# Kernel optimization log

Measured on AMD Instinct MI355X. Metric: run time of the kernel, lower is better.

Reference implementation:

```python
import jax, jax.numpy as jnp
import numpy as np

# atom_dict indices
N_IDX, CA_IDX, C_IDX = 0, 1, 2
O4P_IDX, C2P_IDX, C1P_IDX = 11, 14, 15
NA_REF_IDX = 15  # C1'
TOP_K = 30
NUM_RBF = 16
MAX_REL = 32
NUM_POLY = 3
B, L, A = 1, 512, 24


def setup_inputs() -> dict:
    key = jax.random.key(0)
    ks = jax.random.split(key, 8)
    X = 5.0 * jax.random.normal(ks[0], (B, L, A, 3), dtype=jnp.float32)
    mask = jnp.ones((B, L), dtype=jnp.float32)
    R_idx = jnp.broadcast_to(jnp.arange(L, dtype=jnp.int32), (B, L))
    chain_labels = jnp.broadcast_to((jnp.arange(L) // (L // 2)).astype(jnp.int32), (B, L))
    X_m = jnp.ones((B, L, A), dtype=jnp.float32)
    R_polymer_type = jax.random.randint(ks[1], (B, L), 0, NUM_POLY)
    protein_mask = (R_polymer_type == 0).astype(jnp.float32)
    dna_mask = (R_polymer_type == 1).astype(jnp.float32)
    rna_mask = (R_polymer_type == 2).astype(jnp.float32)
    TOTAL_ATOMS = A + 2
    edge_in = 2 * MAX_REL + 2  # placeholder; real edge_in below
    edge_in = NUM_RBF * TOTAL_ATOMS * TOTAL_ATOMS + 16  # 10832
    W_pos = 0.1 * jax.random.normal(ks[2], (16, 2 * MAX_REL + 2), dtype=jnp.float32)
    b_pos = 0.01 * jax.random.normal(ks[3], (16,), dtype=jnp.float32)
    W_edge = 0.02 * jax.random.normal(ks[4], (128, edge_in), dtype=jnp.float32)
    W_node = 0.1 * jax.random.normal(ks[5], (128, NUM_POLY), dtype=jnp.float32)
    gamma_e = jnp.ones((128,), jnp.float32); beta_e = jnp.zeros((128,), jnp.float32)
    gamma_n = jnp.ones((128,), jnp.float32); beta_n = jnp.zeros((128,), jnp.float32)
    return dict(X=X, mask=mask, R_idx=R_idx, chain_labels=chain_labels, X_m=X_m,
                protein_mask=protein_mask, dna_mask=dna_mask, rna_mask=rna_mask,
                R_polymer_type=R_polymer_type, W_pos=W_pos, b_pos=b_pos,
                W_edge=W_edge, W_node=W_node, gamma_e=gamma_e, beta_e=beta_e,
                gamma_n=gamma_n, beta_n=beta_n)


def _get_cb(n, ca, c, wa, wb, wc):
    b = ca - n
    cc = c - ca
    a = jnp.cross(b, cc)
    return wa * a + wb * b + wc * cc + ca


def _layernorm(x, g, b, eps=1e-5):
    m = x.mean(-1, keepdims=True)
    v = ((x - m) ** 2).mean(-1, keepdims=True)
    return (x - m) / jnp.sqrt(v + eps) * g + b


def _dist_topk(Xc, mask):
    # Xc: [B,L,3]
    mask2d = mask[:, None, :] * mask[:, :, None]  # [B,L,L]
    dX = Xc[:, None, :, :] - Xc[:, :, None, :]
    D = mask2d * jnp.sqrt((dX ** 2).sum(-1) + 1e-6)
    D_max = D.max(-1, keepdims=True)
    D_adjust = D + (1.0 - mask2d) * D_max
    negD, E_idx = jax.lax.top_k(-D_adjust, TOP_K)  # smallest distances
    return -negD, E_idx


def reference(X, mask, R_idx, chain_labels, X_m, protein_mask, dna_mask, rna_mask,
              R_polymer_type, W_pos, b_pos, W_edge, W_node, gamma_e, beta_e,
              gamma_n, beta_n):
    Bb, Ll = X.shape[0], X.shape[1]
    Ca = X[:, :, CA_IDX]
    Nb = X[:, :, N_IDX]
    Cc = X[:, :, C_IDX]
    Cb = _get_cb(Nb, Ca, Cc, -0.58273431, 0.56802827, -0.54067466)
    na_ref = X[:, :, NA_REF_IDX]
    N_na = _get_cb(X[:, :, O4P_IDX], X[:, :, C1P_IDX], X[:, :, C2P_IDX],
                   -0.56967352, 0.51055973, -0.53122153)
    aug_X = jnp.concatenate([X, Cb[:, :, None, :], N_na[:, :, None, :]], axis=2)  # [B,L,26,3]
    aug_Xm = jnp.concatenate([X_m, protein_mask[:, :, None],
                              (rna_mask + dna_mask)[:, :, None]], axis=-1)  # [B,L,26]

    _, E_idx = _dist_topk(Ca + na_ref, mask)  # [B,L,K]

    # gather neighbor atoms / masks: [B,L,K,26,3], [B,L,K,26]
    bidx = jnp.arange(Bb)[:, None, None]
    X_g = aug_X[bidx, E_idx]
    Xm_g = aug_Xm[bidx, E_idx]

    # all-atom pairwise distances [B,L,K,26,26]
    Dall = jnp.sqrt(((aug_X[:, :, None, :, None, :] - X_g[:, :, :, None, :, :]) ** 2).sum(-1) + 1e-6)
    D_mu = jnp.linspace(2.0, 22.0, NUM_RBF)
    D_sigma = (22.0 - 2.0) / NUM_RBF
    RBF = jnp.exp(-((Dall[..., None] - D_mu) / D_sigma) ** 2)  # [B,L,K,26,26,16]
    RBF = RBF * aug_Xm[:, :, None, :, None, None] * Xm_g[:, :, :, None, :, None]
    RBF_all = RBF.reshape(Bb, Ll, TOP_K, -1)  # [B,L,K,26*26*16]

    offset = R_idx[:, :, None] - R_idx[:, None, :]  # [B,L,L]
    offset = jnp.take_along_axis(offset, E_idx, axis=2)  # [B,L,K]
    d_chains = (chain_labels[:, :, None] == chain_labels[:, None, :]).astype(jnp.int32)
    E_chains = jnp.take_along_axis(d_chains, E_idx, axis=2)

    d = jnp.clip(offset + MAX_REL, 0, 2 * MAX_REL) * E_chains + (1 - E_chains) * (2 * MAX_REL + 1)
    d_onehot = jax.nn.one_hot(d, 2 * MAX_REL + 2, dtype=jnp.float32)
    E_positional = d_onehot @ W_pos.T + b_pos  # [B,L,K,16]

    E = jnp.concatenate([E_positional, RBF_all], axis=-1)
    E = E @ W_edge.T  # [B,L,K,128]
    E = _layernorm(E, gamma_e, beta_e)

    V = jax.nn.one_hot(R_polymer_type, NUM_POLY, dtype=jnp.float32) @ W_node.T
    V = _layernorm(V, gamma_n, beta_n)
    return V, E, E_idx
```

## Files before the change

### kernel.cpp

```cpp
#include <hip/hip_runtime.h>
#include <stdint.h>


#define NRES   512
#define TOPK   30
#define NATOM  26
#define KTOT   10832
#define NBLK128 85
#define MTOT   (NRES*TOPK)
#define NOUT   128
#define KSPLIT 6
#define TBINS  1024
#define TRANGE 25.6f

#define OFF_AUGX4  0u
#define OFF_EIDX   212992u
#define OFF_WSWZ   274432u
#define OFF_EPART  1667072u
#define OFF_TAB    25260032u

#define OUT_V     0
#define OUT_E     (NRES*NOUT)
#define OUT_EIDX  (OUT_E + MTOT*NOUT)

typedef __attribute__((ext_vector_type(4))) float f32x4;
typedef __attribute__((ext_vector_type(8))) int   i32x8;

#define SA_C    0.96089792702915984f
#define MU0_C   1.9217958540583197f
#define MUS_C   1.2811972360388798f
#define MUS2_C  (MUS_C*MUS_C)
#define SCL1    0x7f7f7f7f
#define TSCL    (SA_C * (float)TBINS / TRANGE)

__device__ __forceinline__ unsigned short f2bf(float f) {
    unsigned u = __builtin_bit_cast(unsigned, f);
    return (unsigned short)((u + 0x7fffu + ((u >> 16) & 1u)) >> 16);
}
__device__ __forceinline__ float bf2f(unsigned short u) {
    return __builtin_bit_cast(float, (unsigned)u << 16);
}
__device__ __forceinline__ float bflo(unsigned u) {
    return __builtin_bit_cast(float, u << 16);
}
__device__ __forceinline__ float bfhi(unsigned u) {
    return __builtin_bit_cast(float, u & 0xffff0000u);
}
__device__ __forceinline__ unsigned long long shfl_xor_u64(unsigned long long v, int m) {
    unsigned lo = (unsigned)v, hi = (unsigned)(v >> 32);
    lo = (unsigned)__shfl_xor((int)lo, m, 64);
    hi = (unsigned)__shfl_xor((int)hi, m, 64);
    return ((unsigned long long)hi << 32) | lo;
}
__device__ __forceinline__ float fexp2(float x) { return __builtin_amdgcn_exp2f(x); }
__device__ __forceinline__ float fsqrtf(float x) { return __builtin_amdgcn_sqrtf(x); }

__device__ __forceinline__ uint4 lut16(const uint4* __restrict__ tabS,
                                       float4 xi, float jx, float jy, float jz) {
    float dx = xi.x - jx, dy = xi.y - jy, dz = xi.z - jz;
    float d2 = __builtin_fmaf(dx, dx, __builtin_fmaf(dy, dy,
               __builtin_fmaf(dz, dz, 1e-6f)));
    float fi = fsqrtf(d2) * TSCL;
    fi = fminf(fi, (float)(TBINS - 1));
    int idx = (xi.w == 0.0f) ? (TBINS - 1) : (int)fi;
    return tabS[idx];
}

__global__ __launch_bounds__(256) void kPrep(
    const float* __restrict__ X, const float* __restrict__ Xm,
    const float* __restrict__ prot, const float* __restrict__ dna,
    const float* __restrict__ rna, const int* __restrict__ ptype,
    const float* __restrict__ Wn, const float* __restrict__ gn,
    const float* __restrict__ bn, const float* __restrict__ We,
    char* __restrict__ ws, float* __restrict__ out)
{
    if (blockIdx.x >= NRES + 384) {
        int bb = (blockIdx.x - (NRES + 384)) * 256 + threadIdx.x;
        if (bb >= TBINS) return;
        float Ds = ((float)bb + 0.5f) * (TRANGE / (float)TBINS);
        unsigned r[4];
        #pragma unroll
        for (int g = 0; g < 4; g++) {
            float u0 = Ds - (MU0_C + (float)(4*g + 0) * MUS_C);
            float u1 = Ds - (MU0_C + (float)(4*g + 1) * MUS_C);
            float u2 = Ds - (MU0_C + (float)(4*g + 2) * MUS_C);
            float u3 = Ds - (MU0_C + (float)(4*g + 3) * MUS_C);
            float e0 = fexp2(-(u0 * u0));
            float e1 = fexp2(-(u1 * u1));
            float e2 = fexp2(-(u2 * u2));
            float e3 = fexp2(-(u3 * u3));
            int p = __builtin_amdgcn_cvt_pk_fp8_f32(e0, e1, 0, false);
            p     = __builtin_amdgcn_cvt_pk_fp8_f32(e2, e3, p, true);
            r[g] = (unsigned)p;
        }
        *(uint4*)(ws + OFF_TAB + (size_t)bb * 16) =
            make_uint4(r[0], r[1], r[2], r[3]);
        return;
    }
    if (blockIdx.x >= NRES) {
        int idx = blockIdx.x - NRES;
        int n = idx / 3;
        int s = (idx - n*3)*256 + threadIdx.x;
        if (s >= 677) return;
        const float* src = We + (size_t)n*KTOT + ((s < 676) ? (16 + s*16) : 0);
        float4 v0 = ((const float4*)src)[0];
        float4 v1 = ((const float4*)src)[1];
        float4 v2 = ((const float4*)src)[2];
        float4 v3 = ((const float4*)src)[3];
        int d = s >> 3, sl = s & 7, qd2 = sl >> 1, cc = sl & 1;
        size_t base = OFF_WSWZ
                    + (((size_t)(d*8 + (n >> 4))*64) + (size_t)(qd2*16 + (n & 15)))*32
                    + (size_t)cc*16;
        int r0 = __builtin_amdgcn_cvt_pk_fp8_f32(v0.x, v0.y, 0, false);
        r0     = __builtin_amdgcn_cvt_pk_fp8_f32(v0.z, v0.w, r0, true);
        int r1 = __builtin_amdgcn_cvt_pk_fp8_f32(v1.x, v1.y, 0, false);
        r1     = __builtin_amdgcn_cvt_pk_fp8_f32(v1.z, v1.w, r1, true);
        int r2 = __builtin_amdgcn_cvt_pk_fp8_f32(v2.x, v2.y, 0, false);
        r2     = __builtin_amdgcn_cvt_pk_fp8_f32(v2.z, v2.w, r2, true);
        int r3 = __builtin_amdgcn_cvt_pk_fp8_f32(v3.x, v3.y, 0, false);
        r3     = __builtin_amdgcn_cvt_pk_fp8_f32(v3.z, v3.w, r3, true);
        *(uint4*)(ws + base) = make_uint4((unsigned)r0, (unsigned)r1,
                                          (unsigned)r2, (unsigned)r3);
        return;
    }

    const int i = blockIdx.x, t = threadIdx.x;
    if (t >= 128) return;
    float4* augX4 = (float4*)(ws + OFF_AUGX4);
    int*    Eidx  = (int*)(ws + OFF_EIDX);
    const float* Xi = X + i * 72;

    if (t < 26) {
        float x, y, z, mk;
        if (t < 24) {
            x = Xi[t*3]; y = Xi[t*3+1]; z = Xi[t*3+2];
            mk = Xm[i*24 + t];
        } else if (t == 24) {
            float b0 = Xi[3]-Xi[0], b1 = Xi[4]-Xi[1], b2 = Xi[5]-Xi[2];
            float c0 = Xi[6]-Xi[3], c1 = Xi[7]-Xi[4], c2 = Xi[8]-Xi[5];
            float a0 = b1*c2-b2*c1, a1 = b2*c0-b0*c2, a2 = b0*c1-b1*c0;
            x = -0.58273431f*a0 + 0.56802827f*b0 - 0.54067466f*c0 + Xi[3];
            y = -0.58273431f*a1 + 0.56802827f*b1 - 0.54067466f*c1 + Xi[4];
            z = -0.58273431f*a2 + 0.56802827f*b2 - 0.54067466f*c2 + Xi[5];
            mk = prot[i];
        } else {
            const float* O4 = Xi + 33; const float* C1 = Xi + 45; const float* C2 = Xi + 42;
            float b0 = C1[0]-O4[0], b1 = C1[1]-O4[1], b2 = C1[2]-O4[2];
            float c0 = C2[0]-C1[0], c1 = C2[1]-C1[1], c2 = C2[2]-C1[2];
            float a0 = b1*c2-b2*c1, a1 = b2*c0-b0*c2, a2 = b0*c1-b1*c0;
            x = -0.56967352f*a0 + 0.51055973f*b0 - 0.53122153f*c0 + C1[0];
            y = -0.56967352f*a1 + 0.51055973f*b1 - 0.53122153f*c1 + C1[1];
            z = -0.56967352f*a2 + 0.51055973f*b2 - 0.53122153f*c2 + C1[2];
            mk = dna[i] + rna[i];
        }
        augX4[i*26 + t] = make_float4(x, y, z, mk);
    }

    __shared__ float red[4];
    int ty = ptype[i];
    float v = Wn[t*3 + ty];
    float s = v;
    #pragma unroll
    for (int off = 32; off; off >>= 1) s += __shfl_xor(s, off, 64);
    if ((t & 63) == 0) red[t>>6] = s;
    __syncthreads();
    float mean = (red[0] + red[1]) * (1.0f/128.0f);
    float d = v - mean;
    float s2 = d*d;
    #pragma unroll
    for (int off = 32; off; off >>= 1) s2 += __shfl_xor(s2, off, 64);
    if ((t & 63) == 0) red[2 + (t>>6)] = s2;
    __syncthreads();
    float var = (red[2] + red[3]) * (1.0f/128.0f);
    out[OUT_V + i*NOUT + t] = d * rsqrtf(var + 1e-5f) * gn[t] + bn[t];

    if (t >= 64) return;
    const int l = t;
    float xi0 = Xi[3] + Xi[45], xi1 = Xi[4] + Xi[46], xi2 = Xi[5] + Xi[47];
    unsigned long long cand[8];
    #pragma unroll
    for (int sg = 0; sg < 8; sg++) {
        int j = sg*64 + l;
        const float* Xj = X + j*72;
        float c0 = Xj[3] + Xj[45], c1 = Xj[4] + Xj[46], c2 = Xj[5] + Xj[47];
        float dx = xi0 - c0, dy = xi1 - c1, dz = xi2 - c2;
        float dd = __fadd_rn(__fadd_rn(__fadd_rn(__fmul_rn(dx,dx), __fmul_rn(dy,dy)),
                                       __fmul_rn(dz,dz)), 1e-6f);
        float D = sqrtf(dd);
        cand[sg] = ((unsigned long long)__builtin_bit_cast(unsigned, D) << 32) | (unsigned)j;
    }
    for (int m = 0; m < TOPK; m++) {
        unsigned long long k = cand[0];
        #pragma unroll
        for (int sg = 1; sg < 8; sg++) if (cand[sg] < k) k = cand[sg];
        #pragma unroll
        for (int off = 32; off; off >>= 1) {
            unsigned long long o = shfl_xor_u64(k, off);
            if (o < k) k = o;
        }
        if (l == 0) {
            int j = (int)(k & 0xffffffffu);
            Eidx[i*TOPK + m] = j;
            out[OUT_EIDX + i*TOPK + m] = (float)j;
        }
        #pragma unroll
        for (int sg = 0; sg < 8; sg++) if (cand[sg] == k) cand[sg] = ~0ull;
    }
}

__global__ __launch_bounds__(128, 3) void kC(const int* __restrict__ Ridx,
                                             const int* __restrict__ chain,
                                             const float* __restrict__ Wp,
                                             const float* __restrict__ bp,
                                             char* __restrict__ ws)
{
    const int bx = blockIdx.x, q = blockIdx.y;
    const int t = threadIdx.x, lane = t & 63, w = t >> 6;
    const int mlane = lane & 15, qd = lane >> 4;

    const float4* augX4 = (const float4*)(ws + OFF_AUGX4);
    const int*    Eidx  = (const int*)(ws + OFF_EIDX);
    unsigned short* Ep  = (unsigned short*)(ws + OFF_EPART)
                        + (size_t)q * MTOT * NOUT;

    __shared__ uint2  jT[NATOM * 65];
    __shared__ float4 iT[5 * 26];
    __shared__ int    JrowS[64];
    __shared__ uint4  tabS[TBINS];

    if (t < 64) JrowS[t] = Eidx[bx*64 + t];
    __syncthreads();
    const int i_base = (bx*64) / TOPK;
    if (t < 5*26) {
        int il = t / 26, aa = t - il*26;
        int gi = i_base + il; gi = gi > 511 ? 511 : gi;
        iT[t] = augX4[(size_t)gi*26 + aa];
    }
    {
        const uint4* tabG = (const uint4*)(ws + OFF_TAB);
        #pragma unroll
        for (int k = 0; k < 8; k++) tabS[t + k*128] = tabG[t + k*128];
    }
    for (int wk = t; wk < NATOM*64; wk += 128) {
        int aa = wk >> 6, rl = wk & 63;
        float4 p = augX4[(size_t)JrowS[rl]*26 + aa];
        float x = p.x, y = p.y, z = p.z;
        if (p.w == 0.0f) { x = -30000.0f; y = -30000.0f; z = -30000.0f; }
        uint2 pk;
        pk.x = (unsigned)f2bf(x) | ((unsigned)f2bf(y) << 16);
        pk.y = (unsigned)f2bf(z);
        jT[aa*65 + rl] = pk;
    }
    __syncthreads();

    const int rl0 = w*32 + mlane, rl1 = rl0 + 16;
    const int r0 = bx*64 + rl0, r1 = r0 + 16;
    const int i0 = r0 / TOPK, i1 = r1 / TOPK;
    const int il0 = (i0 - i_base)*26, il1 = (i1 - i_base)*26;

    f32x4 acc0[8], acc1[8];
    #pragma unroll
    for (int nt = 0; nt < 8; nt++) {
        acc0[nt] = (f32x4){0.f,0.f,0.f,0.f};
        acc1[nt] = (f32x4){0.f,0.f,0.f,0.f};
    }

    const int d0 = (q == 0) ? 0 : (1 + q*14);
    const int nmain = (q == 0) ? 15 : ((q == 5) ? 13 : 14);

    int s0i = d0*8 + 2*qd;
    int a = s0i / 26, rem = s0i - a*26;

    const char* Wb = (const char*)(ws + OFF_WSWZ) + (size_t)d0*16384 + (size_t)lane*32;

    for (int dd = 0; dd < nmain; dd++) {
        i32x8 b0 = *(const i32x8*)(Wb);
        i32x8 b1 = *(const i32x8*)(Wb + 2048);
        i32x8 b2 = *(const i32x8*)(Wb + 4096);
        i32x8 b3 = *(const i32x8*)(Wb + 6144);

        int rem1 = rem + 1, a1 = a;
        if (rem1 == 26) { rem1 = 0; a1 = a + 1; }

        uint2 jR0a = jT[rem*65  + rl0], jR0b = jT[rem1*65 + rl0];
        uint2 jR1a = jT[rem*65  + rl1], jR1b = jT[rem1*65 + rl1];
        float4 xiR0a = iT[il0 + a], xiR0b = iT[il0 + a1];
        float4 xiR1a = iT[il1 + a], xiR1b = iT[il1 + a1];

        uint4 p0a = lut16(tabS, xiR0a, bflo(jR0a.x), bfhi(jR0a.x), bflo(jR0a.y));
        uint4 p0b = lut16(tabS, xiR0b, bflo(jR0b.x), bfhi(jR0b.x), bflo(jR0b.y));
        uint4 p1a = lut16(tabS, xiR1a, bflo(jR1a.x), bfhi(jR1a.x), bflo(jR1a.y));
        uint4 p1b = lut16(tabS, xiR1b, bflo(jR1b.x), bfhi(jR1b.x), bflo(jR1b.y));

        i32x8 A0, A1;
        A0[0]=p0a.x; A0[1]=p0a.y; A0[2]=p0a.z; A0[3]=p0a.w;
        A0[4]=p0b.x; A0[5]=p0b.y; A0[6]=p0b.z; A0[7]=p0b.w;
        A1[0]=p1a.x; A1[1]=p1a.y; A1[2]=p1a.z; A1[3]=p1a.w;
        A1[4]=p1b.x; A1[5]=p1b.y; A1[6]=p1b.z; A1[7]=p1b.w;

        acc0[0] = __builtin_amdgcn_mfma_scale_f32_16x16x128_f8f6f4(A0, b0, acc0[0], 0, 0, 0, SCL1, 0, SCL1);
        acc1[0] = __builtin_amdgcn_mfma_scale_f32_16x16x128_f8f6f4(A1, b0, acc1[0], 0, 0, 0, SCL1, 0, SCL1);
        acc0[1] = __builtin_amdgcn_mfma_scale_f32_16x16x128_f8f6f4(A0, b1, acc0[1], 0, 0, 0, SCL1, 0, SCL1);
        acc1[1] = __builtin_amdgcn_mfma_scale_f32_16x16x128_f8f6f4(A1, b1, acc1[1], 0, 0, 0, SCL1, 0, SCL1);
        acc0[2] = __builtin_amdgcn_mfma_scale_f32_16x16x128_f8f6f4(A0, b2, acc0[2], 0, 0, 0, SCL1, 0, SCL1);
        acc1[2] = __builtin_amdgcn_mfma_scale_f32_16x16x128_f8f6f4(A1, b2, acc1[2], 0, 0, 0, SCL1, 0, SCL1);
        acc0[3] = __builtin_amdgcn_mfma_scale_f32_16x16x128_f8f6f4(A0, b3, acc0[3], 0, 0, 0, SCL1, 0, SCL1);
        acc1[3] = __builtin_amdgcn_mfma_scale_f32_16x16x128_f8f6f4(A1, b3, acc1[3], 0, 0, 0, SCL1, 0, SCL1);

        i32x8 b4 = *(const i32x8*)(Wb + 8192);
        i32x8 b5 = *(const i32x8*)(Wb + 10240);
        i32x8 b6 = *(const i32x8*)(Wb + 12288);
        i32x8 b7 = *(const i32x8*)(Wb + 14336);

        acc0[4] = __builtin_amdgcn_mfma_scale_f32_16x16x128_f8f6f4(A0, b4, acc0[4], 0, 0, 0, SCL1, 0, SCL1);
        acc1[4] = __builtin_amdgcn_mfma_scale_f32_16x16x128_f8f6f4(A1, b4, acc1[4], 0, 0, 0, SCL1, 0, SCL1);
        acc0[5] = __builtin_amdgcn_mfma_scale_f32_16x16x128_f8f6f4(A0, b5, acc0[5], 0, 0, 0, SCL1, 0, SCL1);
        acc1[5] = __builtin_amdgcn_mfma_scale_f32_16x16x128_f8f6f4(A1, b5, acc1[5], 0, 0, 0, SCL1, 0, SCL1);
        acc0[6] = __builtin_amdgcn_mfma_scale_f32_16x16x128_f8f6f4(A0, b6, acc0[6], 0, 0, 0, SCL1, 0, SCL1);
        acc1[6] = __builtin_amdgcn_mfma_scale_f32_16x16x128_f8f6f4(A1, b6, acc1[6], 0, 0, 0, SCL1, 0, SCL1);
        acc0[7] = __builtin_amdgcn_mfma_scale_f32_16x16x128_f8f6f4(A0, b7, acc0[7], 0, 0, 0, SCL1, 0, SCL1);
        acc1[7] = __builtin_amdgcn_mfma_scale_f32_16x16x128_f8f6f4(A1, b7, acc1[7], 0, 0, 0, SCL1, 0, SCL1);

        Wb += 16384;
        rem += 8;
        if (rem >= 26) { rem -= 26; a += 1; }
    }

    if (q == 5) {
        i32x8 b0 = *(const i32x8*)(Wb);
        i32x8 b1 = *(const i32x8*)(Wb + 2048);
        i32x8 b2 = *(const i32x8*)(Wb + 4096);
        i32x8 b3 = *(const i32x8*)(Wb + 6144);

        int rem1 = rem + 1, a1 = a;
        if (rem1 == 26) { rem1 = 0; a1 = a + 1; }
        int ac  = a  > 25 ? 25 : a;
        int a1c = a1 > 25 ? 25 : a1;

        uint2 jR0a = jT[rem*65  + rl0], jR0b = jT[rem1*65 + rl0];
        uint2 jR1a = jT[rem*65  + rl1], jR1b = jT[rem1*65 + rl1];
        float4 xiR0a = iT[il0 + ac], xiR0b = iT[il0 + a1c];
        float4 xiR1a = iT[il1 + ac], xiR1b = iT[il1 + a1c];

        uint4 p0a = lut16(tabS, xiR0a, bflo(jR0a.x), bfhi(jR0a.x), bflo(jR0a.y));
        uint4 p0b = lut16(tabS, xiR0b, bflo(jR0b.x), bfhi(jR0b.x), bflo(jR0b.y));
        uint4 p1a = lut16(tabS, xiR1a, bflo(jR1a.x), bfhi(jR1a.x), bflo(jR1a.y));
        uint4 p1b = lut16(tabS, xiR1b, bflo(jR1b.x), bfhi(jR1b.x), bflo(jR1b.y));

        if (qd == 2) {
            int dc0, dc1;
            {
                int j0 = JrowS[rl0], j1 = JrowS[rl1];
                int off  = Ridx[i0] - Ridx[j0];
                int same = (chain[i0] == chain[j0]);
                int dc = off + 32; dc = dc < 0 ? 0 : (dc > 64 ? 64 : dc);
                dc0 = same ? dc : 65;
                off  = Ridx[i1] - Ridx[j1];
                same = (chain[i1] == chain[j1]);
                dc = off + 32; dc = dc < 0 ? 0 : (dc > 64 ? 64 : dc);
                dc1 = same ? dc : 65;
            }
            float e0[16], e1[16];
            #pragma unroll
            for (int f = 0; f < 16; f++) {
                float bv = bp[f];
                e0[f] = Wp[f*66 + dc0] + bv;
                e1[f] = Wp[f*66 + dc1] + bv;
            }
            int u0 = __builtin_amdgcn_cvt_pk_fp8_f32(e0[0], e0[1], 0, false);
            u0     = __builtin_amdgcn_cvt_pk_fp8_f32(e0[2], e0[3], u0, true);
            int u1 = __builtin_amdgcn_cvt_pk_fp8_f32(e0[4], e0[5], 0, false);
            u1     = __builtin_amdgcn_cvt_pk_fp8_f32(e0[6], e0[7], u1, true);
            int u2 = __builtin_amdgcn_cvt_pk_fp8_f32(e0[8], e0[9], 0, false);
            u2     = __builtin_amdgcn_cvt_pk_fp8_f32(e0[10], e0[11], u2, true);
            int u3 = __builtin_amdgcn_cvt_pk_fp8_f32(e0[12], e0[13], 0, false);
            u3     = __builtin_amdgcn_cvt_pk_fp8_f32(e0[14], e0[15], u3, true);
            p0a = make_uint4((unsigned)u0,(unsigned)u1,(unsigned)u2,(unsigned)u3);
            u0 = __builtin_amdgcn_cvt_pk_fp8_f32(e1[0], e1[1], 0, false);
            u0 = __builtin_amdgcn_cvt_pk_fp8_f32(e1[2], e1[3], u0, true);
            u1 = __builtin_amdgcn_cvt_pk_fp8_f32(e1[4], e1[5], 0, false);
            u1 = __builtin_amdgcn_cvt_pk_fp8_f32(e1[6], e1[7], u1, true);
            u2 = __builtin_amdgcn_cvt_pk_fp8_f32(e1[8], e1[9], 0, false);
            u2 = __builtin_amdgcn_cvt_pk_fp8_f32(e1[10], e1[11], u2, true);
            u3 = __builtin_amdgcn_cvt_pk_fp8_f32(e1[12], e1[13], 0, false);
            u3 = __builtin_amdgcn_cvt_pk_fp8_f32(e1[14], e1[15], u3, true);
            p1a = make_uint4((unsigned)u0,(unsigned)u1,(unsigned)u2,(unsigned)u3);
            p0b = make_uint4(0,0,0,0);
            p1b = make_uint4(0,0,0,0);
        }
        if (qd == 3) {
            p0a = make_uint4(0,0,0,0); p0b = make_uint4(0,0,0,0);
            p1a = make_uint4(0,0,0,0); p1b = make_uint4(0,0,0,0);
        }

        i32x8 A0, A1;
        A0[0]=p0a.x; A0[1]=p0a.y; A0[2]=p0a.z; A0[3]=p0a.w;
        A0[4]=p0b.x; A0[5]=p0b.y; A0[6]=p0b.z; A0[7]=p0b.w;
        A1[0]=p1a.x; A1[1]=p1a.y; A1[2]=p1a.z; A1[3]=p1a.w;
        A1[4]=p1b.x; A1[5]=p1b.y; A1[6]=p1b.z; A1[7]=p1b.w;

        acc0[0] = __builtin_amdgcn_mfma_scale_f32_16x16x128_f8f6f4(A0, b0, acc0[0], 0, 0, 0, SCL1, 0, SCL1);
        acc1[0] = __builtin_amdgcn_mfma_scale_f32_16x16x128_f8f6f4(A1, b0, acc1[0], 0, 0, 0, SCL1, 0, SCL1);
        acc0[1] = __builtin_amdgcn_mfma_scale_f32_16x16x128_f8f6f4(A0, b1, acc0[1], 0, 0, 0, SCL1, 0, SCL1);
        acc1[1] = __builtin_amdgcn_mfma_scale_f32_16x16x128_f8f6f4(A1, b1, acc1[1], 0, 0, 0, SCL1, 0, SCL1);
        acc0[2] = __builtin_amdgcn_mfma_scale_f32_16x16x128_f8f6f4(A0, b2, acc0[2], 0, 0, 0, SCL1, 0, SCL1);
        acc1[2] = __builtin_amdgcn_mfma_scale_f32_16x16x128_f8f6f4(A1, b2, acc1[2], 0, 0, 0, SCL1, 0, SCL1);
        acc0[3] = __builtin_amdgcn_mfma_scale_f32_16x16x128_f8f6f4(A0, b3, acc0[3], 0, 0, 0, SCL1, 0, SCL1);
        acc1[3] = __builtin_amdgcn_mfma_scale_f32_16x16x128_f8f6f4(A1, b3, acc1[3], 0, 0, 0, SCL1, 0, SCL1);

        i32x8 b4 = *(const i32x8*)(Wb + 8192);
        i32x8 b5 = *(const i32x8*)(Wb + 10240);
        i32x8 b6 = *(const i32x8*)(Wb + 12288);
        i32x8 b7 = *(const i32x8*)(Wb + 14336);

        acc0[4] = __builtin_amdgcn_mfma_scale_f32_16x16x128_f8f6f4(A0, b4, acc0[4], 0, 0, 0, SCL1, 0, SCL1);
        acc1[4] = __builtin_amdgcn_mfma_scale_f32_16x16x128_f8f6f4(A1, b4, acc1[4], 0, 0, 0, SCL1, 0, SCL1);
        acc0[5] = __builtin_amdgcn_mfma_scale_f32_16x16x128_f8f6f4(A0, b5, acc0[5], 0, 0, 0, SCL1, 0, SCL1);
        acc1[5] = __builtin_amdgcn_mfma_scale_f32_16x16x128_f8f6f4(A1, b5, acc1[5], 0, 0, 0, SCL1, 0, SCL1);
        acc0[6] = __builtin_amdgcn_mfma_scale_f32_16x16x128_f8f6f4(A0, b6, acc0[6], 0, 0, 0, SCL1, 0, SCL1);
        acc1[6] = __builtin_amdgcn_mfma_scale_f32_16x16x128_f8f6f4(A1, b6, acc1[6], 0, 0, 0, SCL1, 0, SCL1);
        acc0[7] = __builtin_amdgcn_mfma_scale_f32_16x16x128_f8f6f4(A0, b7, acc0[7], 0, 0, 0, SCL1, 0, SCL1);
        acc1[7] = __builtin_amdgcn_mfma_scale_f32_16x16x128_f8f6f4(A1, b7, acc1[7], 0, 0, 0, SCL1, 0, SCL1);
    }

    #pragma unroll
    for (int nt = 0; nt < 8; nt++) {
        int col = nt*16 + mlane;
        #pragma unroll
        for (int rr = 0; rr < 4; rr++) {
            int g0 = bx*64 + w*32 + qd*4 + rr;
            Ep[(size_t)g0*NOUT + col]      = f2bf(acc0[nt][rr]);
            Ep[(size_t)(g0+16)*NOUT + col] = f2bf(acc1[nt][rr]);
        }
    }
}

__global__ __launch_bounds__(256) void kD(const float* __restrict__ ge,
                                          const float* __restrict__ be,
                                          char* __restrict__ ws,
                                          float* __restrict__ out)
{
    const unsigned* Ep = (const unsigned*)(ws + OFF_EPART);
    const int t = threadIdx.x, wv = t >> 6, lane = t & 63;
    const int row = blockIdx.x*4 + wv;
    const size_t qs = (size_t)MTOT * 64;
    size_t b = (size_t)row*64 + lane;

    float v0 = 0.f, v1 = 0.f;
    #pragma unroll
    for (int qq = 0; qq < KSPLIT; qq++) {
        unsigned u = Ep[b + (size_t)qq*qs];
        v0 += bf2f((unsigned short)(u & 0xffffu));
        v1 += bf2f((unsigned short)(u >> 16));
    }

    float S = v0 + v1, Q = v0*v0 + v1*v1;
    #pragma unroll
    for (int off = 32; off; off >>= 1) {
        S += __shfl_xor(S, off, 64);
        Q += __shfl_xor(Q, off, 64);
    }
    float mean = S * (1.0f/128.0f);
    float var  = Q * (1.0f/128.0f) - mean*mean;
    float rstd = rsqrtf(var + 1e-5f);
    float2 o;
    o.x = (v0 - mean) * rstd * ge[2*lane]   + be[2*lane];
    o.y = (v1 - mean) * rstd * ge[2*lane+1] + be[2*lane+1];
    ((float2*)(out + OUT_E))[(size_t)row*64 + lane] = o;
}

extern "C" void kernel_launch(void* const* d_in, const int* in_sizes, int n_in,
                              void* d_out, int out_size, void* d_ws, size_t ws_size,
                              hipStream_t stream)
{
    const float* X     = (const float*)d_in[0];
    const int*   Ridx  = (const int*)d_in[2];
    const int*   chain = (const int*)d_in[3];
    const float* Xm    = (const float*)d_in[4];
    const float* prot  = (const float*)d_in[5];
    const float* dna   = (const float*)d_in[6];
    const float* rna   = (const float*)d_in[7];
    const int*   ptype = (const int*)d_in[8];
    const float* Wp    = (const float*)d_in[9];
    const float* bp    = (const float*)d_in[10];
    const float* We    = (const float*)d_in[11];
    const float* Wn    = (const float*)d_in[12];
    const float* ge    = (const float*)d_in[13];
    const float* be    = (const float*)d_in[14];
    const float* gn    = (const float*)d_in[15];
    const float* bn    = (const float*)d_in[16];
    char* ws = (char*)d_ws;
    float* out = (float*)d_out;

    kPrep<<<dim3(NRES + 384 + TBINS/256), dim3(256), 0, stream>>>(X, Xm, prot,
            dna, rna, ptype, Wn, gn, bn, We, ws, out);
    kC<<<dim3(240, KSPLIT), dim3(128), 0, stream>>>(Ridx, chain, Wp, bp, ws);
    kD<<<dim3(MTOT/4), dim3(256), 0, stream>>>(ge, be, ws, out);
}
```

Measured before the change: 168.6 us.

## Fuse split-K partial reduction and edge layernorm into GEMM kernel via LDS

The six split-K slices move from separate blocks into six waves of one 384-thread block. Each wave adds its partial accumulators into a shared-memory tile with atomics, and the block then applies the layernorm and writes the final edge features directly. This removes the bf16 partial-sum buffer in global memory and the separate reduction/layernorm kernel launch, which also avoids the bf16 rounding of the partials. In exchange each block covers only 32 rows, and it pays for LDS atomics and an extra barrier. Occupancy and register pressure also change under the new 384-thread launch bounds.

Result: slower. 216.7 us (+28.5%).

```diff
diff --git a/kernel.cpp b/kernel.cpp
--- a/kernel.cpp
+++ b/kernel.cpp
@@ -9,15 +9,13 @@
 #define NBLK128 85
 #define MTOT   (NRES*TOPK)
 #define NOUT   128
-#define KSPLIT 6
 #define TBINS  1024
 #define TRANGE 25.6f
 
 #define OFF_AUGX4  0u
 #define OFF_EIDX   212992u
 #define OFF_WSWZ   274432u
-#define OFF_EPART  1667072u
-#define OFF_TAB    25260032u
+#define OFF_TAB    1667072u
 
 #define OUT_V     0
 #define OUT_E     (NRES*NOUT)
@@ -36,9 +34,6 @@
 __device__ __forceinline__ unsigned short f2bf(float f) {
     unsigned u = __builtin_bit_cast(unsigned, f);
     return (unsigned short)((u + 0x7fffu + ((u >> 16) & 1u)) >> 16);
-}
-__device__ __forceinline__ float bf2f(unsigned short u) {
-    return __builtin_bit_cast(float, (unsigned)u << 16);
 }
 __device__ __forceinline__ float bflo(unsigned u) {
     return __builtin_bit_cast(float, u << 16);
@@ -208,53 +203,55 @@
     }
 }
 
-__global__ __launch_bounds__(128, 3) void kC(const int* __restrict__ Ridx,
+__global__ __launch_bounds__(384, 2) void kC(const int* __restrict__ Ridx,
                                              const int* __restrict__ chain,
                                              const float* __restrict__ Wp,
                                              const float* __restrict__ bp,
-                                             char* __restrict__ ws)
+                                             const float* __restrict__ ge,
+                                             const float* __restrict__ be,
+                                             char* __restrict__ ws,
+                                             float* __restrict__ out)
 {
-    const int bx = blockIdx.x, q = blockIdx.y;
+    const int bx = blockIdx.x;
     const int t = threadIdx.x, lane = t & 63, w = t >> 6;
     const int mlane = lane & 15, qd = lane >> 4;
 
     const float4* augX4 = (const float4*)(ws + OFF_AUGX4);
     const int*    Eidx  = (const int*)(ws + OFF_EIDX);
-    unsigned short* Ep  = (unsigned short*)(ws + OFF_EPART)
-                        + (size_t)q * MTOT * NOUT;
-
-    __shared__ uint2  jT[NATOM * 65];
-    __shared__ float4 iT[5 * 26];
-    __shared__ int    JrowS[64];
+
+    __shared__ uint2  jT[NATOM * 33];
+    __shared__ float4 iT[3 * 26];
+    __shared__ int    JrowS[32];
     __shared__ uint4  tabS[TBINS];
-
-    if (t < 64) JrowS[t] = Eidx[bx*64 + t];
+    __shared__ float  accS[32 * 132];
+
+    if (t < 32) JrowS[t] = Eidx[bx*32 + t];
+    for (int k = t; k < 32*132; k += 384) accS[k] = 0.0f;
     __syncthreads();
-    const int i_base = (bx*64) / TOPK;
-    if (t < 5*26) {
+    const int i_base = (bx*32) / TOPK;
+    if (t < 3*26) {
         int il = t / 26, aa = t - il*26;
         int gi = i_base + il; gi = gi > 511 ? 511 : gi;
         iT[t] = augX4[(size_t)gi*26 + aa];
     }
     {
         const uint4* tabG = (const uint4*)(ws + OFF_TAB);
-        #pragma unroll
-        for (int k = 0; k < 8; k++) tabS[t + k*128] = tabG[t + k*128];
-    }
-    for (int wk = t; wk < NATOM*64; wk += 128) {
-        int aa = wk >> 6, rl = wk & 63;
+        for (int k = t; k < TBINS; k += 384) tabS[k] = tabG[k];
+    }
+    for (int wk = t; wk < NATOM*32; wk += 384) {
+        int aa = wk >> 5, rl = wk & 31;
         float4 p = augX4[(size_t)JrowS[rl]*26 + aa];
         float x = p.x, y = p.y, z = p.z;
         if (p.w == 0.0f) { x = -30000.0f; y = -30000.0f; z = -30000.0f; }
         uint2 pk;
         pk.x = (unsigned)f2bf(x) | ((unsigned)f2bf(y) << 16);
         pk.y = (unsigned)f2bf(z);
-        jT[aa*65 + rl] = pk;
+        jT[aa*33 + rl] = pk;
     }
     __syncthreads();
 
-    const int rl0 = w*32 + mlane, rl1 = rl0 + 16;
-    const int r0 = bx*64 + rl0, r1 = r0 + 16;
+    const int rl0 = mlane, rl1 = mlane + 16;
+    const int r0 = bx*32 + rl0, r1 = r0 + 16;
     const int i0 = r0 / TOPK, i1 = r1 / TOPK;
     const int il0 = (i0 - i_base)*26, il1 = (i1 - i_base)*26;
 
@@ -265,6 +262,7 @@
         acc1[nt] = (f32x4){0.f,0.f,0.f,0.f};
     }
 
+    const int q = w;
     const int d0 = (q == 0) ? 0 : (1 + q*14);
     const int nmain = (q == 0) ? 15 : ((q == 5) ? 13 : 14);
 
@@ -282,8 +280,8 @@
         int rem1 = rem + 1, a1 = a;
         if (rem1 == 26) { rem1 = 0; a1 = a + 1; }
 
-        uint2 jR0a = jT[rem*65  + rl0], jR0b = jT[rem1*65 + rl0];
-        uint2 jR1a = jT[rem*65  + rl1], jR1b = jT[rem1*65 + rl1];
+        uint2 jR0a = jT[rem*33  + rl0], jR0b = jT[rem1*33 + rl0];
+        uint2 jR1a = jT[rem*33  + rl1], jR1b = jT[rem1*33 + rl1];
         float4 xiR0a = iT[il0 + a], xiR0b = iT[il0 + a1];
         float4 xiR1a = iT[il1 + a], xiR1b = iT[il1 + a1];
 
@@ -337,8 +335,8 @@
         int ac  = a  > 25 ? 25 : a;
         int a1c = a1 > 25 ? 25 : a1;
 
-        uint2 jR0a = jT[rem*65  + rl0], jR0b = jT[rem1*65 + rl0];
-        uint2 jR1a = jT[rem*65  + rl1], jR1b = jT[rem1*65 + rl1];
+        uint2 jR0a = jT[rem*33  + rl0], jR0b = jT[rem1*33 + rl0];
+        uint2 jR1a = jT[rem*33  + rl1], jR1b = jT[rem1*33 + rl1];
         float4 xiR0a = iT[il0 + ac], xiR0b = iT[il0 + a1c];
         float4 xiR1a = iT[il1 + ac], xiR1b = iT[il1 + a1c];
 
@@ -428,45 +426,30 @@
         int col = nt*16 + mlane;
         #pragma unroll
         for (int rr = 0; rr < 4; rr++) {
-            int g0 = bx*64 + w*32 + qd*4 + rr;
-            Ep[(size_t)g0*NOUT + col]      = f2bf(acc0[nt][rr]);
-            Ep[(size_t)(g0+16)*NOUT + col] = f2bf(acc1[nt][rr]);
-        }
-    }
-}
-
-__global__ __launch_bounds__(256) void kD(const float* __restrict__ ge,
-                                          const float* __restrict__ be,
-                                          char* __restrict__ ws,
-                                          float* __restrict__ out)
-{
-    const unsigned* Ep = (const unsigned*)(ws + OFF_EPART);
-    const int t = threadIdx.x, wv = t >> 6, lane = t & 63;
-    const int row = blockIdx.x*4 + wv;
-    const size_t qs = (size_t)MTOT * 64;
-    size_t b = (size_t)row*64 + lane;
-
-    float v0 = 0.f, v1 = 0.f;
-    #pragma unroll
-    for (int qq = 0; qq < KSPLIT; qq++) {
-        unsigned u = Ep[b + (size_t)qq*qs];
-        v0 += bf2f((unsigned short)(u & 0xffffu));
-        v1 += bf2f((unsigned short)(u >> 16));
-    }
-
-    float S = v0 + v1, Q = v0*v0 + v1*v1;
-    #pragma unroll
-    for (int off = 32; off; off >>= 1) {
-        S += __shfl_xor(S, off, 64);
-        Q += __shfl_xor(Q, off, 64);
-    }
-    float mean = S * (1.0f/128.0f);
-    float var  = Q * (1.0f/128.0f) - mean*mean;
-    float rstd = rsqrtf(var + 1e-5f);
-    float2 o;
-    o.x = (v0 - mean) * rstd * ge[2*lane]   + be[2*lane];
-    o.y = (v1 - mean) * rstd * ge[2*lane+1] + be[2*lane+1];
-    ((float2*)(out + OUT_E))[(size_t)row*64 + lane] = o;
+            int r = qd*4 + rr;
+            atomicAdd(&accS[r*132 + col],        acc0[nt][rr]);
+            atomicAdd(&accS[(r+16)*132 + col],   acc1[nt][rr]);
+        }
+    }
+    __syncthreads();
+
+    for (int r = w; r < 32; r += 6) {
+        float v0 = accS[r*132 + 2*lane];
+        float v1 = accS[r*132 + 2*lane + 1];
+        float S = v0 + v1, Q = v0*v0 + v1*v1;
+        #pragma unroll
+        for (int off = 32; off; off >>= 1) {
+            S += __shfl_xor(S, off, 64);
+            Q += __shfl_xor(Q, off, 64);
+        }
+        float mean = S * (1.0f/128.0f);
+        float var  = Q * (1.0f/128.0f) - mean*mean;
+        float rstd = rsqrtf(var + 1e-5f);
+        float2 o;
+        o.x = (v0 - mean) * rstd * ge[2*lane]   + be[2*lane];
+        o.y = (v1 - mean) * rstd * ge[2*lane+1] + be[2*lane+1];
+        ((float2*)(out + OUT_E))[(size_t)(bx*32 + r)*64 + lane] = o;
+    }
 }
 
 extern "C" void kernel_launch(void* const* d_in, const int* in_sizes, int n_in,
@@ -494,6 +477,6 @@
 
     kPrep<<<dim3(NRES + 384 + TBINS/256), dim3(256), 0, stream>>>(X, Xm, prot,
             dna, rna, ptype, Wn, gn, bn, We, ws, out);
-    kC<<<dim3(240, KSPLIT), dim3(128), 0, stream>>>(Ridx, chain, Wp, bp, ws);
-    kD<<<dim3(MTOT/4), dim3(256), 0, stream>>>(ge, be, ws, out);
-}
+    kC<<<dim3(MTOT/32), dim3(384), 0, stream>>>(Ridx, chain, Wp, bp, ge, be,
+            ws, out);
+}
```

## Split warp work by output columns instead of rows in fp8 MFMA GEMM

Applied to the files above, without the earlier changes.

Each of the two waves now covers all 64 rows of the block and half of the 128 output columns, instead of 32 rows by all 128 columns. Each wave loads only 4 weight fragments per step rather than 8, which halves per-wave global weight traffic. In exchange each wave computes the LUT-based RBF A-fragments for four row tiles instead of two, so the gather and LUT work per wave doubles. Accumulator register count stays the same.

After: 162.8 us. 3.4% less time.

```diff
diff --git a/kernel.cpp b/kernel.cpp
--- a/kernel.cpp
+++ b/kernel.cpp
@@ -232,8 +232,8 @@
     __syncthreads();
     const int i_base = (bx*64) / TOPK;
     if (t < 5*26) {
-        int il = t / 26, aa = t - il*26;
-        int gi = i_base + il; gi = gi > 511 ? 511 : gi;
+        int il_ = t / 26, aa = t - il_*26;
+        int gi = i_base + il_; gi = gi > 511 ? 511 : gi;
         iT[t] = augX4[(size_t)gi*26 + aa];
     }
     {
@@ -242,28 +242,30 @@
         for (int k = 0; k < 8; k++) tabS[t + k*128] = tabG[t + k*128];
     }
     for (int wk = t; wk < NATOM*64; wk += 128) {
-        int aa = wk >> 6, rl = wk & 63;
-        float4 p = augX4[(size_t)JrowS[rl]*26 + aa];
+        int aa = wk >> 6, rl_ = wk & 63;
+        float4 p = augX4[(size_t)JrowS[rl_]*26 + aa];
         float x = p.x, y = p.y, z = p.z;
         if (p.w == 0.0f) { x = -30000.0f; y = -30000.0f; z = -30000.0f; }
         uint2 pk;
         pk.x = (unsigned)f2bf(x) | ((unsigned)f2bf(y) << 16);
         pk.y = (unsigned)f2bf(z);
-        jT[aa*65 + rl] = pk;
+        jT[aa*65 + rl_] = pk;
     }
     __syncthreads();
 
-    const int rl0 = w*32 + mlane, rl1 = rl0 + 16;
-    const int r0 = bx*64 + rl0, r1 = r0 + 16;
-    const int i0 = r0 / TOPK, i1 = r1 / TOPK;
-    const int il0 = (i0 - i_base)*26, il1 = (i1 - i_base)*26;
-
-    f32x4 acc0[8], acc1[8];
-    #pragma unroll
-    for (int nt = 0; nt < 8; nt++) {
-        acc0[nt] = (f32x4){0.f,0.f,0.f,0.f};
-        acc1[nt] = (f32x4){0.f,0.f,0.f,0.f};
-    }
+    int rl[4], il[4];
+    #pragma unroll
+    for (int rt = 0; rt < 4; rt++) {
+        rl[rt] = rt*16 + mlane;
+        il[rt] = ((bx*64 + rl[rt]) / TOPK - i_base) * 26;
+    }
+
+    f32x4 acc[4][4];
+    #pragma unroll
+    for (int rt = 0; rt < 4; rt++)
+        #pragma unroll
+        for (int nt = 0; nt < 4; nt++)
+            acc[rt][nt] = (f32x4){0.f,0.f,0.f,0.f};
 
     const int d0 = (q == 0) ? 0 : (1 + q*14);
     const int nmain = (q == 0) ? 15 : ((q == 5) ? 13 : 14);
@@ -271,7 +273,8 @@
     int s0i = d0*8 + 2*qd;
     int a = s0i / 26, rem = s0i - a*26;
 
-    const char* Wb = (const char*)(ws + OFF_WSWZ) + (size_t)d0*16384 + (size_t)lane*32;
+    const char* Wb = (const char*)(ws + OFF_WSWZ) + (size_t)d0*16384
+                   + (size_t)(w*4)*2048 + (size_t)lane*32;
 
     for (int dd = 0; dd < nmain; dd++) {
         i32x8 b0 = *(const i32x8*)(Wb);
@@ -282,44 +285,22 @@
         int rem1 = rem + 1, a1 = a;
         if (rem1 == 26) { rem1 = 0; a1 = a + 1; }
 
-        uint2 jR0a = jT[rem*65  + rl0], jR0b = jT[rem1*65 + rl0];
-        uint2 jR1a = jT[rem*65  + rl1], jR1b = jT[rem1*65 + rl1];
-        float4 xiR0a = iT[il0 + a], xiR0b = iT[il0 + a1];
-        float4 xiR1a = iT[il1 + a], xiR1b = iT[il1 + a1];
-
-        uint4 p0a = lut16(tabS, xiR0a, bflo(jR0a.x), bfhi(jR0a.x), bflo(jR0a.y));
-        uint4 p0b = lut16(tabS, xiR0b, bflo(jR0b.x), bfhi(jR0b.x), bflo(jR0b.y));
-        uint4 p1a = lut16(tabS, xiR1a, bflo(jR1a.x), bfhi(jR1a.x), bflo(jR1a.y));
-        uint4 p1b = lut16(tabS, xiR1b, bflo(jR1b.x), bfhi(jR1b.x), bflo(jR1b.y));
-
-        i32x8 A0, A1;
-        A0[0]=p0a.x; A0[1]=p0a.y; A0[2]=p0a.z; A0[3]=p0a.w;
-        A0[4]=p0b.x; A0[5]=p0b.y; A0[6]=p0b.z; A0[7]=p0b.w;
-        A1[0]=p1a.x; A1[1]=p1a.y; A1[2]=p1a.z; A1[3]=p1a.w;
-        A1[4]=p1b.x; A1[5]=p1b.y; A1[6]=p1b.z; A1[7]=p1b.w;
-
-        acc0[0] = __builtin_amdgcn_mfma_scale_f32_16x16x128_f8f6f4(A0, b0, acc0[0], 0, 0, 0, SCL1, 0, SCL1);
-        acc1[0] = __builtin_amdgcn_mfma_scale_f32_16x16x128_f8f6f4(A1, b0, acc1[0], 0, 0, 0, SCL1, 0, SCL1);
-        acc0[1] = __builtin_amdgcn_mfma_scale_f32_16x16x128_f8f6f4(A0, b1, acc0[1], 0, 0, 0, SCL1, 0, SCL1);
-        acc1[1] = __builtin_amdgcn_mfma_scale_f32_16x16x128_f8f6f4(A1, b1, acc1[1], 0, 0, 0, SCL1, 0, SCL1);
-        acc0[2] = __builtin_amdgcn_mfma_scale_f32_16x16x128_f8f6f4(A0, b2, acc0[2], 0, 0, 0, SCL1, 0, SCL1);
-        acc1[2] = __builtin_amdgcn_mfma_scale_f32_16x16x128_f8f6f4(A1, b2, acc1[2], 0, 0, 0, SCL1, 0, SCL1);
-        acc0[3] = __builtin_amdgcn_mfma_scale_f32_16x16x128_f8f6f4(A0, b3, acc0[3], 0, 0, 0, SCL1, 0, SCL1);
-        acc1[3] = __builtin_amdgcn_mfma_scale_f32_16x16x128_f8f6f4(A1, b3, acc1[3], 0, 0, 0, SCL1, 0, SCL1);
-
-        i32x8 b4 = *(const i32x8*)(Wb + 8192);
-        i32x8 b5 = *(const i32x8*)(Wb + 10240);
-        i32x8 b6 = *(const i32x8*)(Wb + 12288);
-        i32x8 b7 = *(const i32x8*)(Wb + 14336);
-
-        acc0[4] = __builtin_amdgcn_mfma_scale_f32_16x16x128_f8f6f4(A0, b4, acc0[4], 0, 0, 0, SCL1, 0, SCL1);
-        acc1[4] = __builtin_amdgcn_mfma_scale_f32_16x16x128_f8f6f4(A1, b4, acc1[4], 0, 0, 0, SCL1, 0, SCL1);
-        acc0[5] = __builtin_amdgcn_mfma_scale_f32_16x16x128_f8f6f4(A0, b5, acc0[5], 0, 0, 0, SCL1, 0, SCL1);
-        acc1[5] = __builtin_amdgcn_mfma_scale_f32_16x16x128_f8f6f4(A1, b5, acc1[5], 0, 0, 0, SCL1, 0, SCL1);
-        acc0[6] = __builtin_amdgcn_mfma_scale_f32_16x16x128_f8f6f4(A0, b6, acc0[6], 0, 0, 0, SCL1, 0, SCL1);
-        acc1[6] = __builtin_amdgcn_mfma_scale_f32_16x16x128_f8f6f4(A1, b6, acc1[6], 0, 0, 0, SCL1, 0, SCL1);
-        acc0[7] = __builtin_amdgcn_mfma_scale_f32_16x16x128_f8f6f4(A0, b7, acc0[7], 0, 0, 0, SCL1, 0, SCL1);
-        acc1[7] = __builtin_amdgcn_mfma_scale_f32_16x16x128_f8f6f4(A1, b7, acc1[7], 0, 0, 0, SCL1, 0, SCL1);
+        #pragma unroll
+        for (int rt = 0; rt < 4; rt++) {
+            uint2 ja = jT[rem*65  + rl[rt]];
+            uint2 jb = jT[rem1*65 + rl[rt]];
+            float4 xa = iT[il[rt] + a];
+            float4 xb = iT[il[rt] + a1];
+            uint4 pa = lut16(tabS, xa, bflo(ja.x), bfhi(ja.x), bflo(ja.y));
+            uint4 pb = lut16(tabS, xb, bflo(jb.x), bfhi(jb.x), bflo(jb.y));
+            i32x8 A;
+            A[0]=pa.x; A[1]=pa.y; A[2]=pa.z; A[3]=pa.w;
+            A[4]=pb.x; A[5]=pb.y; A[6]=pb.z; A[7]=pb.w;
+            acc[rt][0] = __builtin_amdgcn_mfma_scale_f32_16x16x128_f8f6f4(A, b0, acc[rt][0], 0, 0, 0, SCL1, 0, SCL1);
+            acc[rt][1] = __builtin_amdgcn_mfma_scale_f32_16x16x128_f8f6f4(A, b1, acc[rt][1], 0, 0, 0, SCL1, 0, SCL1);
+            acc[rt][2] = __builtin_amdgcn_mfma_scale_f32_16x16x128_f8f6f4(A, b2, acc[rt][2], 0, 0, 0, SCL1, 0, SCL1);
+            acc[rt][3] = __builtin_amdgcn_mfma_scale_f32_16x16x128_f8f6f4(A, b3, acc[rt][3], 0, 0, 0, SCL1, 0, SCL1);
+        }
 
         Wb += 16384;
         rem += 8;
@@ -337,100 +318,69 @@
         int ac  = a  > 25 ? 25 : a;
         int a1c = a1 > 25 ? 25 : a1;
 
-        uint2 jR0a = jT[rem*65  + rl0], jR0b = jT[rem1*65 + rl0];
-        uint2 jR1a = jT[rem*65  + rl1], jR1b = jT[rem1*65 + rl1];
-        float4 xiR0a = iT[il0 + ac], xiR0b = iT[il0 + a1c];
-        float4 xiR1a = iT[il1 + ac], xiR1b = iT[il1 + a1c];
-
-        uint4 p0a = lut16(tabS, xiR0a, bflo(jR0a.x), bfhi(jR0a.x), bflo(jR0a.y));
-        uint4 p0b = lut16(tabS, xiR0b, bflo(jR0b.x), bfhi(jR0b.x), bflo(jR0b.y));
-        uint4 p1a = lut16(tabS, xiR1a, bflo(jR1a.x), bfhi(jR1a.x), bflo(jR1a.y));
-        uint4 p1b = lut16(tabS, xiR1b, bflo(jR1b.x), bfhi(jR1b.x), bflo(jR1b.y));
-
+        int dcv[4];
         if (qd == 2) {
-            int dc0, dc1;
-            {
-                int j0 = JrowS[rl0], j1 = JrowS[rl1];
-                int off  = Ridx[i0] - Ridx[j0];
-                int same = (chain[i0] == chain[j0]);
+            #pragma unroll
+            for (int rt = 0; rt < 4; rt++) {
+                int j  = JrowS[rl[rt]];
+                int i_ = (bx*64 + rl[rt]) / TOPK;
+                int off  = Ridx[i_] - Ridx[j];
+                int same = (chain[i_] == chain[j]);
                 int dc = off + 32; dc = dc < 0 ? 0 : (dc > 64 ? 64 : dc);
-                dc0 = same ? dc : 65;
-                off  = Ridx[i1] - Ridx[j1];
-                same = (chain[i1] == chain[j1]);
-                dc = off + 32; dc = dc < 0 ? 0 : (dc > 64 ? 64 : dc);
-                dc1 = same ? dc : 65;
+                dcv[rt] = same ? dc : 65;
             }
-            float e0[16], e1[16];
+        }
+
+        #pragma unroll
+        for (int rt = 0; rt < 4; rt++) {
+            uint2 ja = jT[rem*65  + rl[rt]];
+            uint2 jb = jT[rem1*65 + rl[rt]];
+            float4 xa = iT[il[rt] + ac];
+            float4 xb = iT[il[rt] + a1c];
+            uint4 pa = lut16(tabS, xa, bflo(ja.x), bfhi(ja.x), bflo(ja.y));
+            uint4 pb = lut16(tabS, xb, bflo(jb.x), bfhi(jb.x), bflo(jb.y));
+
+            if (qd == 2) {
+                float e[16];
+                #pragma unroll
+                for (int f = 0; f < 16; f++)
+                    e[f] = Wp[f*66 + dcv[rt]] + bp[f];
+                int u0 = __builtin_amdgcn_cvt_pk_fp8_f32(e[0], e[1], 0, false);
+                u0     = __builtin_amdgcn_cvt_pk_fp8_f32(e[2], e[3], u0, true);
+                int u1 = __builtin_amdgcn_cvt_pk_fp8_f32(e[4], e[5], 0, false);
+                u1     = __builtin_amdgcn_cvt_pk_fp8_f32(e[6], e[7], u1, true);
+                int u2 = __builtin_amdgcn_cvt_pk_fp8_f32(e[8], e[9], 0, false);
+                u2     = __builtin_amdgcn_cvt_pk_fp8_f32(e[10], e[11], u2, true);
+                int u3 = __builtin_amdgcn_cvt_pk_fp8_f32(e[12], e[13], 0, false);
+                u3     = __builtin_amdgcn_cvt_pk_fp8_f32(e[14], e[15], u3, true);
+                pa = make_uint4((unsigned)u0,(unsigned)u1,(unsigned)u2,(unsigned)u3);
+                pb = make_uint4(0,0,0,0);
+            }
+            if (qd == 3) {
+                pa = make_uint4(0,0,0,0);
+                pb = make_uint4(0,0,0,0);
+            }
+
+            i32x8 A;
+            A[0]=pa.x; A[1]=pa.y; A[2]=pa.z; A[3]=pa.w;
+            A[4]=pb.x; A[5]=pb.y; A[6]=pb.z; A[7]=pb.w;
+            acc[rt][0] = __builtin_amdgcn_mfma_scale_f32_16x16x128_f8f6f4(A, b0, acc[rt][0], 0, 0, 0, SCL1, 0, SCL1);
+            acc[rt][1] = __builtin_amdgcn_mfma_scale_f32_16x16x128_f8f6f4(A, b1, acc[rt][1], 0, 0, 0, SCL1, 0, SCL1);
+            acc[rt][2] = __builtin_amdgcn_mfma_scale_f32_16x16x128_f8f6f4(A, b2, acc[rt][2], 0, 0, 0, SCL1, 0, SCL1);
+            acc[rt][3] = __builtin_amdgcn_mfma_scale_f32_16x16x128_f8f6f4(A, b3, acc[rt][3], 0, 0, 0, SCL1, 0, SCL1);
+        }
+    }
+
+    #pragma unroll
+    for (int rt = 0; rt < 4; rt++) {
+        #pragma unroll
+        for (int nt = 0; nt < 4; nt++) {
+            int col = (w*4 + nt)*16 + mlane;
             #pragma unroll
-            for (int f = 0; f < 16; f++) {
-                float bv = bp[f];
-                e0[f] = Wp[f*66 + dc0] + bv;
-                e1[f] = Wp[f*66 + dc1] + bv;
+            for (int rr = 0; rr < 4; rr++) {
+                int g0 = bx*64 + rt*16 + qd*4 + rr;
+                Ep[(size_t)g0*NOUT + col] = f2bf(acc[rt][nt][rr]);
             }
-            int u0 = __builtin_amdgcn_cvt_pk_fp8_f32(e0[0], e0[1], 0, false);
-            u0     = __builtin_amdgcn_cvt_pk_fp8_f32(e0[2], e0[3], u0, true);
-            int u1 = __builtin_amdgcn_cvt_pk_fp8_f32(e0[4], e0[5], 0, false);
-            u1     = __builtin_amdgcn_cvt_pk_fp8_f32(e0[6], e0[7], u1, true);
-            int u2 = __builtin_amdgcn_cvt_pk_fp8_f32(e0[8], e0[9], 0, false);
-            u2     = __builtin_amdgcn_cvt_pk_fp8_f32(e0[10], e0[11], u2, true);
-            int u3 = __builtin_amdgcn_cvt_pk_fp8_f32(e0[12], e0[13], 0, false);
-            u3     = __builtin_amdgcn_cvt_pk_fp8_f32(e0[14], e0[15], u3, true);
-            p0a = make_uint4((unsigned)u0,(unsigned)u1,(unsigned)u2,(unsigned)u3);
-            u0 = __builtin_amdgcn_cvt_pk_fp8_f32(e1[0], e1[1], 0, false);
-            u0 = __builtin_amdgcn_cvt_pk_fp8_f32(e1[2], e1[3], u0, true);
-            u1 = __builtin_amdgcn_cvt_pk_fp8_f32(e1[4], e1[5], 0, false);
-            u1 = __builtin_amdgcn_cvt_pk_fp8_f32(e1[6], e1[7], u1, true);
-            u2 = __builtin_amdgcn_cvt_pk_fp8_f32(e1[8], e1[9], 0, false);
-            u2 = __builtin_amdgcn_cvt_pk_fp8_f32(e1[10], e1[11], u2, true);
-            u3 = __builtin_amdgcn_cvt_pk_fp8_f32(e1[12], e1[13], 0, false);
-            u3 = __builtin_amdgcn_cvt_pk_fp8_f32(e1[14], e1[15], u3, true);
-            p1a = make_uint4((unsigned)u0,(unsigned)u1,(unsigned)u2,(unsigned)u3);
-            p0b = make_uint4(0,0,0,0);
-            p1b = make_uint4(0,0,0,0);
-        }
-        if (qd == 3) {
-            p0a = make_uint4(0,0,0,0); p0b = make_uint4(0,0,0,0);
-            p1a = make_uint4(0,0,0,0); p1b = make_uint4(0,0,0,0);
-        }
-
-        i32x8 A0, A1;
-        A0[0]=p0a.x; A0[1]=p0a.y; A0[2]=p0a.z; A0[3]=p0a.w;
-        A0[4]=p0b.x; A0[5]=p0b.y; A0[6]=p0b.z; A0[7]=p0b.w;
-        A1[0]=p1a.x; A1[1]=p1a.y; A1[2]=p1a.z; A1[3]=p1a.w;
-        A1[4]=p1b.x; A1[5]=p1b.y; A1[6]=p1b.z; A1[7]=p1b.w;
-
-        acc0[0] = __builtin_amdgcn_mfma_scale_f32_16x16x128_f8f6f4(A0, b0, acc0[0], 0, 0, 0, SCL1, 0, SCL1);
-        acc1[0] = __builtin_amdgcn_mfma_scale_f32_16x16x128_f8f6f4(A1, b0, acc1[0], 0, 0, 0, SCL1, 0, SCL1);
-        acc0[1] = __builtin_amdgcn_mfma_scale_f32_16x16x128_f8f6f4(A0, b1, acc0[1], 0, 0, 0, SCL1, 0, SCL1);
-        acc1[1] = __builtin_amdgcn_mfma_scale_f32_16x16x128_f8f6f4(A1, b1, acc1[1], 0, 0, 0, SCL1, 0, SCL1);
-        acc0[2] = __builtin_amdgcn_mfma_scale_f32_16x16x128_f8f6f4(A0, b2, acc0[2], 0, 0, 0, SCL1, 0, SCL1);
-        acc1[2] = __builtin_amdgcn_mfma_scale_f32_16x16x128_f8f6f4(A1, b2, acc1[2], 0, 0, 0, SCL1, 0, SCL1);
-        acc0[3] = __builtin_amdgcn_mfma_scale_f32_16x16x128_f8f6f4(A0, b3, acc0[3], 0, 0, 0, SCL1, 0, SCL1);
-        acc1[3] = __builtin_amdgcn_mfma_scale_f32_16x16x128_f8f6f4(A1, b3, acc1[3], 0, 0, 0, SCL1, 0, SCL1);
-
-        i32x8 b4 = *(const i32x8*)(Wb + 8192);
-        i32x8 b5 = *(const i32x8*)(Wb + 10240);
-        i32x8 b6 = *(const i32x8*)(Wb + 12288);
-        i32x8 b7 = *(const i32x8*)(Wb + 14336);
-
-        acc0[4] = __builtin_amdgcn_mfma_scale_f32_16x16x128_f8f6f4(A0, b4, acc0[4], 0, 0, 0, SCL1, 0, SCL1);
-        acc1[4] = __builtin_amdgcn_mfma_scale_f32_16x16x128_f8f6f4(A1, b4, acc1[4], 0, 0, 0, SCL1, 0, SCL1);
-        acc0[5] = __builtin_amdgcn_mfma_scale_f32_16x16x128_f8f6f4(A0, b5, acc0[5], 0, 0, 0, SCL1, 0, SCL1);
-        acc1[5] = __builtin_amdgcn_mfma_scale_f32_16x16x128_f8f6f4(A1, b5, acc1[5], 0, 0, 0, SCL1, 0, SCL1);
-        acc0[6] = __builtin_amdgcn_mfma_scale_f32_16x16x128_f8f6f4(A0, b6, acc0[6], 0, 0, 0, SCL1, 0, SCL1);
-        acc1[6] = __builtin_amdgcn_mfma_scale_f32_16x16x128_f8f6f4(A1, b6, acc1[6], 0, 0, 0, SCL1, 0, SCL1);
-        acc0[7] = __builtin_amdgcn_mfma_scale_f32_16x16x128_f8f6f4(A0, b7, acc0[7], 0, 0, 0, SCL1, 0, SCL1);
-        acc1[7] = __builtin_amdgcn_mfma_scale_f32_16x16x128_f8f6f4(A1, b7, acc1[7], 0, 0, 0, SCL1, 0, SCL1);
-    }
-
-    #pragma unroll
-    for (int nt = 0; nt < 8; nt++) {
-        int col = nt*16 + mlane;
-        #pragma unroll
-        for (int rr = 0; rr < 4; rr++) {
-            int g0 = bx*64 + w*32 + qd*4 + rr;
-            Ep[(size_t)g0*NOUT + col]      = f2bf(acc0[nt][rr]);
-            Ep[(size_t)(g0+16)*NOUT + col] = f2bf(acc1[nt][rr]);
         }
     }
 }
```
